# Performance work log

Measured on AMD Instinct MI355X. Metric: run time of the kernel, lower is better.

The kernel has to match this reference:

```python
import jax, jax.numpy as jnp
import numpy as np

B, L, C = 128, 512, 321
PRED = 336
S = 4
K = 25  # moving_avg kernel
EPS = 1e-5
N = L // S          # 128
H = 2048 // S       # 512


def setup_inputs() -> dict:
    key = jax.random.key(0)
    ks = jax.random.split(key, 16)
    def w(k, shape, fan_in):
        return jax.random.uniform(k, shape, jnp.float32, -1.0, 1.0) / np.sqrt(fan_in)
    return {
        "x": jax.random.normal(ks[0], (B, L, C), jnp.float32),
        "revin_w": jnp.ones((C,), jnp.float32),
        "revin_b": jnp.zeros((C,), jnp.float32),
        "W11": w(ks[1], (N, H), N), "b11": w(ks[2], (H,), N),
        "W12": w(ks[3], (H, N), H), "b12": w(ks[4], (N,), H),
        "W21": w(ks[5], (N, H), N), "b21": w(ks[6], (H,), N),
        "W22": w(ks[7], (H, N), H), "b22": w(ks[8], (N,), H),
        "W_tr": w(ks[9], (L, PRED), L), "b_tr": w(ks[10], (PRED,), L),
        "W_se": w(ks[11], (L, PRED), L), "b_se": w(ks[12], (PRED,), L),
    }


def reference(x, revin_w, revin_b, W11, b11, W12, b12, W21, b21, W22, b22,
              W_tr, b_tr, W_se, b_se):
    # RevIN norm (statistics are detached in the original)
    mean = jax.lax.stop_gradient(jnp.mean(x, axis=1, keepdims=True))
    std = jax.lax.stop_gradient(
        jnp.sqrt(jnp.var(x, axis=1, keepdims=True) + EPS))
    xn = (x - mean) / std * revin_w + revin_b  # [B, L, C]

    # Decomp: replicate-pad along time then moving average of width K
    front = jnp.repeat(xn[:, 0:1, :], K - 1 - (K - 1) // 2, axis=1)
    end = jnp.repeat(xn[:, -1:, :], (K - 1) // 2, axis=1)
    padded = jnp.concatenate([front, xn, end], axis=1)  # [B, L+K-1, C]
    cs = jnp.concatenate(
        [jnp.zeros((B, 1, C), padded.dtype), jnp.cumsum(padded, axis=1)], axis=1)
    trend = (cs[:, K:, :] - cs[:, :-K, :]) / K  # [B, L, C]
    seasonal = xn - trend

    trend_p = jnp.transpose(trend, (0, 2, 1))      # [B, C, L]
    seasonal_p = jnp.transpose(seasonal, (0, 2, 1))  # [B, C, L]

    # Trend head: Linear L -> PRED
    trend_out = jnp.einsum('bcl,lp->bcp', trend_p, W_tr) + b_tr

    # Seasonal head: Splitting (strided interleave) = reshape + transpose
    xs = seasonal_p.reshape(B, C, N, S).transpose(0, 1, 3, 2)  # [B, C, S, N]
    h = jnp.matmul(jax.nn.gelu(jnp.matmul(xs, W11) + b11, approximate=False), W12) + b12
    h = jnp.matmul(jax.nn.gelu(jnp.matmul(h, W21) + b21, approximate=False), W22) + b22
    # Catting is the exact inverse interleave
    sea = h.transpose(0, 1, 3, 2).reshape(B, C, L)  # [B, C, L]
    sea_out = jnp.einsum('bcl,lp->bcp', sea, W_se) + b_se

    out = jnp.transpose(trend_out + sea_out, (0, 2, 1))  # [B, PRED, C]

    # RevIN denorm
    out = (out - revin_b) / (revin_w + EPS * EPS)
    out = out * std + mean
    return out
```

## Files before the change

kernel.cpp:

```cpp
#include <hip/hip_runtime.h>
#include <math.h>

#define BB   128
#define LL   512
#define CC   321
#define PREDD 336

using bf16x8  = __attribute__((ext_vector_type(8))) __bf16;
using floatx4 = __attribute__((ext_vector_type(4))) float;
using uintx4  = __attribute__((ext_vector_type(4))) unsigned int;
typedef unsigned short u16;

__device__ __forceinline__ u16 f2bf(float f){
    union { float f; unsigned u; } v; v.f = f;
    unsigned r = v.u + 0x7FFFu + ((v.u >> 16) & 1u);
    return (u16)(r >> 16);
}

__device__ __forceinline__ float fgelu(float x){
    float u = x*(0.7978845608f + 0.035677408f*x*x);
    float a = fminf(u*2.8853900818f, 80.f);
    float t = __builtin_amdgcn_exp2f(a);
    return x*t*__builtin_amdgcn_rcpf(1.f + t);
}

__global__ void prep_k(const float* __restrict__ W11, const float* __restrict__ W12,
                       const float* __restrict__ W21, const float* __restrict__ W22,
                       const float* __restrict__ Wtr, const float* __restrict__ Wse,
                       u16* __restrict__ BT1, u16* __restrict__ BT2,
                       u16* __restrict__ BT3, u16* __restrict__ BT4,
                       u16* __restrict__ BT5)
{
    int idx = blockIdx.x * 256 + threadIdx.x;
    if (idx < 65536){
        int h = idx >> 7, k = idx & 127;
        BT1[idx] = f2bf(W11[k*512 + h]);
        BT3[idx] = f2bf(W21[k*512 + h]);
        int n = idx >> 9, k2 = idx & 511;
        BT2[idx] = f2bf(W12[k2*128 + n]);
        BT4[idx] = f2bf(W22[k2*128 + n]);
    }
    if (idx < 393216){
        int p = idx >> 10, k = idx & 1023;
        float v = 0.f;
        if (p < PREDD){
            if (k < 512) v = Wtr[k*PREDD + p];
            else { int kk = k - 512; int s = kk >> 7; int n = kk & 127; v = Wse[(4*n + s)*PREDD + p]; }
        }
        BT5[idx] = f2bf(v);
    }
}

#define XT(t,c) xt[((t)<<4) + (((t)>>5)<<1) + (c)]
__global__ __launch_bounds__(256) void decomp_k(
    const float* __restrict__ x, const float* __restrict__ rw, const float* __restrict__ rb,
    u16* __restrict__ Afin, u16* __restrict__ xs, float2* __restrict__ stats)
{
    __shared__ float xt[8240];
    __shared__ float red[2][16][16];
    __shared__ float sh_m[16], sh_istd[16];
    int b = blockIdx.x / 21, ct = blockIdx.x % 21;
    int tid = threadIdx.x;

    int cl = tid & 15, lp = tid >> 4;
    int c = ct*16 + cl;
    bool valid = c < CC;
    const float* xb = x + (size_t)b*LL*CC;
    float s = 0.f, q = 0.f;
    for (int i = 0; i < 32; ++i){
        int t = lp + 16*i;
        float v = valid ? xb[(size_t)t*CC + c] : 0.f;
        XT(t, cl) = v;
        s += v; q += v*v;
    }
    red[0][lp][cl] = s; red[1][lp][cl] = q;
    __syncthreads();
    if (tid < 16){
        float ss = 0.f, qq = 0.f;
        for (int j = 0; j < 16; ++j){ ss += red[0][j][tid]; qq += red[1][j][tid]; }
        float m  = ss * (1.f/512.f);
        float var = qq * (1.f/512.f) - m*m;
        float sd = sqrtf(var + 1e-5f);
        sh_m[tid] = m; sh_istd[tid] = 1.f/sd;
        int cc = ct*16 + tid;
        if (cc < CC) stats[(size_t)b*CC + cc] = make_float2(m, sd);
    }
    __syncthreads();

    int ch = tid >> 4, tp = tid & 15;
    int c2 = ct*16 + ch;
    if (c2 >= CC) return;
    float m = sh_m[ch], istd = sh_istd[ch];
    float w = rw[c2] * istd, bbv = rb[c2];
    size_t bc = (size_t)b*CC + c2;
    u16* tr  = Afin + bc*1024;
    u16* xsr = xs   + bc*512;
    int t0 = tp*32;

    float win = 0.f;
#pragma unroll
    for (int d = -12; d <= 12; ++d){
        int u = t0 + d; u = u < 0 ? 0 : (u > 511 ? 511 : u);
        win += XT(u, ch);
    }
    u16 trbuf[8];
    u16 xsbuf[4][8];
#pragma unroll
    for (int i = 0; i < 32; ++i){
        int t = t0 + i;
        float Ax = win * (1.f/25.f);
        float xv = XT(t, ch);
        trbuf[i & 7] = f2bf((Ax - m)*w + bbv);
        xsbuf[i & 3][i >> 2] = f2bf((xv - Ax)*w);
        if ((i & 7) == 7)
            *(uintx4*)(tr + t0 + (i & ~7)) = *(const uintx4*)trbuf;
        int uo = t - 12; uo = uo < 0 ? 0 : uo;
        int un = t + 13; un = un > 511 ? 511 : un;
        win += XT(un, ch) - XT(uo, ch);
    }
#pragma unroll
    for (int s4 = 0; s4 < 4; ++s4)
        *(uintx4*)(xsr + s4*128 + tp*8) = *(const uintx4*)xsbuf[s4];
}

#define SA 136
#define SB 72
#define HB0 8704
#define W2B0 17920
__global__ __launch_bounds__(256, 2) void mlp_fused_k(
    const u16* __restrict__ xs,
    const u16* __restrict__ BT1, const float* __restrict__ b11,
    const u16* __restrict__ BT2, const float* __restrict__ b12,
    const u16* __restrict__ BT3, const float* __restrict__ b21,
    const u16* __restrict__ BT4, const float* __restrict__ b22,
    u16* __restrict__ Afin)
{
    __shared__ u16 lds[27136];
    const int tid = threadIdx.x;
    const int row0 = blockIdx.x * 128;
    const int lane = tid & 63;
    const int wv = tid >> 6;
    const int wm = wv & 1, wn = wv >> 1;
    const int quad = lane >> 4, cl = lane & 15;

    {
        int r = tid >> 4, c8 = (tid & 15) * 8;
        const u16* src = xs + (size_t)(row0 + r)*128 + c8;
        u16* dst = lds + r*SA + c8;
#pragma unroll
        for (int p = 0; p < 8; ++p)
            *(uintx4*)(dst + p*16*SA) = *(const uintx4*)(src + (size_t)p*16*128);
    }
    __syncthreads();

    for (int mlp = 0; mlp < 2; ++mlp){
        const u16*  BTa = mlp ? BT3 : BT1;
        const float* ba = mlp ? b21 : b11;
        const u16*  BTb = mlp ? BT4 : BT2;
        const float* bb = mlp ? b22 : b12;

        bf16x8 afrag[4][4];
#pragma unroll
        for (int mt = 0; mt < 4; ++mt)
#pragma unroll
            for (int ks = 0; ks < 4; ++ks)
                afrag[mt][ks] = *(const bf16x8*)(lds + (wm*64 + mt*16 + cl)*SA + ks*32 + quad*8);
        __syncthreads();

        floatx4 Yacc[16];
#pragma unroll
        for (int i = 0; i < 16; ++i) Yacc[i] = (floatx4){0.f,0.f,0.f,0.f};

        for (int hc = 0; hc < 8; ++hc){
            {
                int r = tid >> 4, c8 = (tid & 15) * 8;
                const u16* src = BTa + (size_t)(hc*64 + r)*128 + c8;
                u16* dst = lds + r*SA + c8;
#pragma unroll
                for (int p = 0; p < 4; ++p)
                    *(uintx4*)(dst + p*16*SA) = *(const uintx4*)(src + (size_t)p*16*128);
            }
            __syncthreads();

            floatx4 hacc[8];
#pragma unroll
            for (int i = 0; i < 8; ++i) hacc[i] = (floatx4){0.f,0.f,0.f,0.f};
#pragma unroll
            for (int ks = 0; ks < 4; ++ks){
                bf16x8 bfr0 = *(const bf16x8*)(lds + (wn*32 +  0 + cl)*SA + ks*32 + quad*8);
                bf16x8 bfr1 = *(const bf16x8*)(lds + (wn*32 + 16 + cl)*SA + ks*32 + quad*8);
#pragma unroll
                for (int mt = 0; mt < 4; ++mt){
                    hacc[mt*2+0] = __builtin_amdgcn_mfma_f32_16x16x32_bf16(afrag[mt][ks], bfr0, hacc[mt*2+0], 0, 0, 0);
                    hacc[mt*2+1] = __builtin_amdgcn_mfma_f32_16x16x32_bf16(afrag[mt][ks], bfr1, hacc[mt*2+1], 0, 0, 0);
                }
            }
            {
                int hl0 = wn*32 + cl;
                float bav0 = ba[hc*64 + hl0];
                float bav1 = ba[hc*64 + hl0 + 16];
#pragma unroll
                for (int mt = 0; mt < 4; ++mt){
                    floatx4 v0 = hacc[mt*2+0], v1 = hacc[mt*2+1];
#pragma unroll
                    for (int i = 0; i < 4; ++i){
                        int r = wm*64 + mt*16 + quad*4 + i;
                        lds[HB0 + r*SB + hl0]      = f2bf(fgelu(v0[i] + bav0));
                        lds[HB0 + r*SB + hl0 + 16] = f2bf(fgelu(v1[i] + bav1));
                    }
                }
            }
            {
                int r = tid >> 3, c8 = (tid & 7) * 8;
                const u16* src = BTb + (size_t)r*512 + hc*64 + c8;
                u16* dst = lds + W2B0 + r*SB + c8;
#pragma unroll
                for (int p = 0; p < 4; ++p)
                    *(uintx4*)(dst + p*32*SB) = *(const uintx4*)(src + (size_t)p*32*512);
            }
            __syncthreads();

#pragma unroll
            for (int ks = 0; ks < 2; ++ks){
                bf16x8 a2[4], b2[4];
#pragma unroll
                for (int mt = 0; mt < 4; ++mt) a2[mt] = *(const bf16x8*)(lds + HB0  + (wm*64 + mt*16 + cl)*SB + ks*32 + quad*8);
#pragma unroll
                for (int nt = 0; nt < 4; ++nt) b2[nt] = *(const bf16x8*)(lds + W2B0 + (wn*64 + nt*16 + cl)*SB + ks*32 + quad*8);
#pragma unroll
                for (int mt = 0; mt < 4; ++mt)
#pragma unroll
                    for (int nt = 0; nt < 4; ++nt)
                        Yacc[mt*4+nt] = __builtin_amdgcn_mfma_f32_16x16x32_bf16(a2[mt], b2[nt], Yacc[mt*4+nt], 0, 0, 0);
            }
        }
        __syncthreads();

        if (mlp == 0){
#pragma unroll
            for (int mt = 0; mt < 4; ++mt)
#pragma unroll
                for (int nt = 0; nt < 4; ++nt){
                    int c = wn*64 + nt*16 + cl;
                    float bv = bb[c];
                    floatx4 v = Yacc[mt*4+nt];
#pragma unroll
                    for (int i = 0; i < 4; ++i){
                        int r = wm*64 + mt*16 + quad*4 + i;
                        lds[r*SA + c] = f2bf(v[i] + bv);
                    }
                }
            __syncthreads();
        } else {
#pragma unroll
            for (int mt = 0; mt < 4; ++mt)
#pragma unroll
                for (int nt = 0; nt < 4; ++nt){
                    int c = wn*64 + nt*16 + cl;
                    float bv = bb[c];
                    floatx4 v = Yacc[mt*4+nt];
#pragma unroll
                    for (int i = 0; i < 4; ++i){
                        int gr = row0 + wm*64 + mt*16 + quad*4 + i;
                        Afin[(size_t)(gr>>2)*1024 + 512 + (size_t)(gr&3)*128 + c] = f2bf(v[i] + bv);
                    }
                }
        }
    }
}

__global__ __launch_bounds__(256, 2) void head_gemm_k(
    const u16* __restrict__ A, const u16* __restrict__ BT,
    float* __restrict__ Cf,
    const float* __restrict__ bias, const float* __restrict__ bias2,
    const float* __restrict__ rw, const float* __restrict__ rb,
    const float2* __restrict__ stats)
{
    __shared__ u16 lA[128*72];
    __shared__ u16 lB[128*72];
    const int tid = threadIdx.x;
    const int row0 = blockIdx.y * 128;
    const int col0 = blockIdx.x * 128;
    const int lane = tid & 63;
    const int wv = tid >> 6;
    const int wm = wv & 1, wn = wv >> 1;
    const int quad = lane >> 4, cl = lane & 15;

    floatx4 acc[16];
#pragma unroll
    for (int i = 0; i < 16; ++i) acc[i] = (floatx4){0.f,0.f,0.f,0.f};

    const int srow = tid >> 3, sseg = tid & 7;
    const u16* Ag = A  + (size_t)(row0 + srow)*1024 + sseg*8;
    const u16* Bg = BT + (size_t)(col0 + srow)*1024 + sseg*8;

    for (int k0 = 0; k0 < 1024; k0 += 64){
#pragma unroll
        for (int p = 0; p < 4; ++p){
            uintx4 av = *(const uintx4*)(Ag + (size_t)p*32*1024 + k0);
            uintx4 bv = *(const uintx4*)(Bg + (size_t)p*32*1024 + k0);
            int r = p*32 + srow;
            *(uintx4*)(lA + r*72 + sseg*8) = av;
            *(uintx4*)(lB + r*72 + sseg*8) = bv;
        }
        __syncthreads();
#pragma unroll
        for (int kk = 0; kk < 2; ++kk){
            const int lk = kk*32 + quad*8;
            bf16x8 af[4], bfr[4];
#pragma unroll
            for (int mt = 0; mt < 4; ++mt) af[mt]  = *(const bf16x8*)(lA + (wm*64 + mt*16 + cl)*72 + lk);
#pragma unroll
            for (int nt = 0; nt < 4; ++nt) bfr[nt] = *(const bf16x8*)(lB + (wn*64 + nt*16 + cl)*72 + lk);
#pragma unroll
            for (int mt = 0; mt < 4; ++mt)
#pragma unroll
                for (int nt = 0; nt < 4; ++nt)
                    acc[mt*4+nt] = __builtin_amdgcn_mfma_f32_16x16x32_bf16(af[mt], bfr[nt], acc[mt*4+nt], 0, 0, 0);
        }
        __syncthreads();
    }

#pragma unroll
    for (int mt = 0; mt < 4; ++mt)
#pragma unroll
        for (int nt = 0; nt < 4; ++nt){
            floatx4 v = acc[mt*4+nt];
            int gc = col0 + wn*64 + nt*16 + cl;
            if (gc >= PREDD) continue;
            float bsum = bias[gc] + bias2[gc];
#pragma unroll
            for (int i = 0; i < 4; ++i){
                int gr = row0 + wm*64 + mt*16 + quad*4 + i;
                float val = v[i] + bsum;
                int bv2 = gr / CC;
                int c  = gr - bv2*CC;
                val = (val - rb[c]) / (rw[c] + 1e-10f);
                float2 st = stats[gr];
                val = val*st.y + st.x;
                Cf[(size_t)bv2*(PREDD*CC) + (size_t)gc*CC + c] = val;
            }
        }
}

extern "C" void kernel_launch(void* const* d_in, const int* in_sizes, int n_in,
                              void* d_out, int out_size, void* d_ws, size_t ws_size,
                              hipStream_t stream)
{
    const float* x   = (const float*)d_in[0];
    const float* rvw = (const float*)d_in[1];
    const float* rvb = (const float*)d_in[2];
    const float* W11 = (const float*)d_in[3];
    const float* b11 = (const float*)d_in[4];
    const float* W12 = (const float*)d_in[5];
    const float* b12 = (const float*)d_in[6];
    const float* W21 = (const float*)d_in[7];
    const float* b21 = (const float*)d_in[8];
    const float* W22 = (const float*)d_in[9];
    const float* b22 = (const float*)d_in[10];
    const float* Wtr = (const float*)d_in[11];
    const float* btr = (const float*)d_in[12];
    const float* Wse = (const float*)d_in[13];
    const float* bse = (const float*)d_in[14];
    float* out = (float*)d_out;

    char* ws = (char*)d_ws;
    u16* BT1 = (u16*)(ws + 0);
    u16* BT2 = (u16*)(ws + 131072);
    u16* BT3 = (u16*)(ws + 262144);
    u16* BT4 = (u16*)(ws + 393216);
    u16* BT5 = (u16*)(ws + 524288);
    float2* stats = (float2*)(ws + 1310720);
    u16* Afin = (u16*)(ws + 1639424);
    u16* xs   = (u16*)(ws + 85787648);

    hipLaunchKernelGGL(prep_k, dim3(1536), dim3(256), 0, stream,
                       W11, W12, W21, W22, Wtr, Wse, BT1, BT2, BT3, BT4, BT5);
    hipLaunchKernelGGL(decomp_k, dim3(128*21), dim3(256), 0, stream,
                       x, rvw, rvb, Afin, xs, stats);
    hipLaunchKernelGGL(mlp_fused_k, dim3(1284), dim3(256), 0, stream,
                       xs, BT1, b11, BT2, b12, BT3, b21, BT4, b22, Afin);
    hipLaunchKernelGGL(head_gemm_k, dim3(3, 321), dim3(256), 0, stream,
                       Afin, BT5, out, btr, bse, rvw, rvb, stats);
}
```

Measured before the change: 523.1 us.

## Software-pipeline weight loads and swizzle LDS in MLP and head GEMM kernels

The fused MLP kernel now prefetches the next hidden chunk's W1/W2 tiles into registers while computing. It double-buffers the GELU output and W2 tiles so the second GEMM of one chunk overlaps the first GEMM of the next. Padded LDS strides are replaced with XOR-swizzled layouts to avoid bank conflicts without padding. The head GEMM gets the same register prefetch and swizzle, with launch bounds raised to 3 blocks per CU, which adds register pressure and larger LDS use in the MLP kernel.

```diff
diff --git a/kernel.cpp b/kernel.cpp
--- a/kernel.cpp
+++ b/kernel.cpp
@@ -10,6 +10,8 @@
 using floatx4 = __attribute__((ext_vector_type(4))) float;
 using uintx4  = __attribute__((ext_vector_type(4))) unsigned int;
 typedef unsigned short u16;
+
+#define MFMA16(a,b,c) __builtin_amdgcn_mfma_f32_16x16x32_bf16(a,b,c,0,0,0)
 
 __device__ __forceinline__ u16 f2bf(float f){
     union { float f; unsigned u; } v; v.f = f;
@@ -23,6 +25,9 @@
     float t = __builtin_amdgcn_exp2f(a);
     return x*t*__builtin_amdgcn_rcpf(1.f + t);
 }
+
+__device__ __forceinline__ int swz128(int r, int s){ return r*128 + (((s & 8) | ((s ^ r) & 7)) << 3); }
+__device__ __forceinline__ int swz64 (int r, int s){ return r*64  + (((s ^ r) & 7) << 3); }
 
 __global__ void prep_k(const float* __restrict__ W11, const float* __restrict__ W12,
                        const float* __restrict__ W21, const float* __restrict__ W22,
@@ -123,10 +128,8 @@
         *(uintx4*)(xsr + s4*128 + tp*8) = *(const uintx4*)xsbuf[s4];
 }
 
-#define SA 136
-#define SB 72
-#define HB0 8704
-#define W2B0 17920
+#define W1B 16384
+#define W2B 24576
 __global__ __launch_bounds__(256, 2) void mlp_fused_k(
     const u16* __restrict__ xs,
     const u16* __restrict__ BT1, const float* __restrict__ b11,
@@ -135,7 +138,7 @@
     const u16* __restrict__ BT4, const float* __restrict__ b22,
     u16* __restrict__ Afin)
 {
-    __shared__ u16 lds[27136];
+    __shared__ u16 lds[40960];
     const int tid = threadIdx.x;
     const int row0 = blockIdx.x * 128;
     const int lane = tid & 63;
@@ -143,20 +146,26 @@
     const int wm = wv & 1, wn = wv >> 1;
     const int quad = lane >> 4, cl = lane & 15;
 
+    const int r1 = tid >> 2, s1 = tid & 3;
+    const int r2 = tid >> 1, s2 = (tid & 1)*4;
+
+    uintx4 w1r[4], w2r[4];
+#pragma unroll
+    for (int p = 0; p < 4; ++p){
+        w1r[p] = *(const uintx4*)(BT1 + (size_t)r1*128 + (s1 + 4*p)*8);
+        w2r[p] = *(const uintx4*)(BT2 + (size_t)r2*512 + (s2 + p)*8);
+    }
     {
-        int r = tid >> 4, c8 = (tid & 15) * 8;
-        const u16* src = xs + (size_t)(row0 + r)*128 + c8;
-        u16* dst = lds + r*SA + c8;
+        int rr = tid >> 4, seg = tid & 15;
+        const u16* src = xs + (size_t)(row0 + rr)*128 + seg*8;
 #pragma unroll
         for (int p = 0; p < 8; ++p)
-            *(uintx4*)(dst + p*16*SA) = *(const uintx4*)(src + (size_t)p*16*128);
+            *(uintx4*)(lds + swz128(rr + p*16, seg)) = *(const uintx4*)(src + (size_t)p*16*128);
     }
     __syncthreads();
 
     for (int mlp = 0; mlp < 2; ++mlp){
-        const u16*  BTa = mlp ? BT3 : BT1;
         const float* ba = mlp ? b21 : b11;
-        const u16*  BTb = mlp ? BT4 : BT2;
         const float* bb = mlp ? b22 : b12;
 
         bf16x8 afrag[4][4];
@@ -164,74 +173,105 @@
         for (int mt = 0; mt < 4; ++mt)
 #pragma unroll
             for (int ks = 0; ks < 4; ++ks)
-                afrag[mt][ks] = *(const bf16x8*)(lds + (wm*64 + mt*16 + cl)*SA + ks*32 + quad*8);
-        __syncthreads();
+                afrag[mt][ks] = *(const bf16x8*)(lds + swz128(wm*64 + mt*16 + cl, ks*4 + quad));
+
+        if (mlp == 0){
+#pragma unroll
+            for (int p = 0; p < 4; ++p){
+                *(uintx4*)(lds + W1B + swz128(r1, s1 + 4*p)) = w1r[p];
+                *(uintx4*)(lds + W2B + swz64(r2, s2 + p))    = w2r[p];
+            }
+        }
 
         floatx4 Yacc[16];
 #pragma unroll
         for (int i = 0; i < 16; ++i) Yacc[i] = (floatx4){0.f,0.f,0.f,0.f};
+        floatx4 hacc[8];
 
         for (int hc = 0; hc < 8; ++hc){
+            const int g = mlp*8 + hc;
+            __syncthreads();
+            if (g < 15){
+                const u16* w1s = ((g+1) & 8) ? BT3 : BT1;
+                const u16* w2s = ((g+1) & 8) ? BT4 : BT2;
+                const int hb = ((g+1) & 7) * 64;
+#pragma unroll
+                for (int p = 0; p < 4; ++p){
+                    w1r[p] = *(const uintx4*)(w1s + (size_t)(hb + r1)*128 + (s1 + 4*p)*8);
+                    w2r[p] = *(const uintx4*)(w2s + (size_t)r2*512 + hb + (s2 + p)*8);
+                }
+            }
+#pragma unroll
+            for (int i = 0; i < 8; ++i) hacc[i] = (floatx4){0.f,0.f,0.f,0.f};
+#pragma unroll
+            for (int ks = 0; ks < 4; ++ks){
+                bf16x8 b0 = *(const bf16x8*)(lds + W1B + swz128(wn*32 + cl,      ks*4 + quad));
+                bf16x8 b1 = *(const bf16x8*)(lds + W1B + swz128(wn*32 + 16 + cl, ks*4 + quad));
+#pragma unroll
+                for (int mt = 0; mt < 4; ++mt){
+                    hacc[mt*2+0] = MFMA16(afrag[mt][ks], b0, hacc[mt*2+0]);
+                    hacc[mt*2+1] = MFMA16(afrag[mt][ks], b1, hacc[mt*2+1]);
+                }
+            }
+            if (hc > 0){
+                const int HBp = ((hc-1) & 1) * 8192;
+                const int W2p = W2B + ((hc-1) & 1) * 8192;
+#pragma unroll
+                for (int ks = 0; ks < 2; ++ks){
+                    bf16x8 a2[4], b2[4];
+#pragma unroll
+                    for (int mt = 0; mt < 4; ++mt) a2[mt] = *(const bf16x8*)(lds + HBp + swz64(wm*64 + mt*16 + cl, ks*4 + quad));
+#pragma unroll
+                    for (int nt = 0; nt < 4; ++nt) b2[nt] = *(const bf16x8*)(lds + W2p + swz64(wn*64 + nt*16 + cl, ks*4 + quad));
+#pragma unroll
+                    for (int mt = 0; mt < 4; ++mt)
+#pragma unroll
+                        for (int nt = 0; nt < 4; ++nt)
+                            Yacc[mt*4+nt] = MFMA16(a2[mt], b2[nt], Yacc[mt*4+nt]);
+                }
+            }
             {
-                int r = tid >> 4, c8 = (tid & 15) * 8;
-                const u16* src = BTa + (size_t)(hc*64 + r)*128 + c8;
-                u16* dst = lds + r*SA + c8;
-#pragma unroll
-                for (int p = 0; p < 4; ++p)
-                    *(uintx4*)(dst + p*16*SA) = *(const uintx4*)(src + (size_t)p*16*128);
-            }
-            __syncthreads();
-
-            floatx4 hacc[8];
-#pragma unroll
-            for (int i = 0; i < 8; ++i) hacc[i] = (floatx4){0.f,0.f,0.f,0.f};
-#pragma unroll
-            for (int ks = 0; ks < 4; ++ks){
-                bf16x8 bfr0 = *(const bf16x8*)(lds + (wn*32 +  0 + cl)*SA + ks*32 + quad*8);
-                bf16x8 bfr1 = *(const bf16x8*)(lds + (wn*32 + 16 + cl)*SA + ks*32 + quad*8);
+                const int HB = (hc & 1) * 8192;
+                int h0 = wn*32 + cl;
+                int h1v = h0 + 16;
+                float bav0 = ba[hc*64 + h0];
+                float bav1 = ba[hc*64 + h1v];
 #pragma unroll
                 for (int mt = 0; mt < 4; ++mt){
-                    hacc[mt*2+0] = __builtin_amdgcn_mfma_f32_16x16x32_bf16(afrag[mt][ks], bfr0, hacc[mt*2+0], 0, 0, 0);
-                    hacc[mt*2+1] = __builtin_amdgcn_mfma_f32_16x16x32_bf16(afrag[mt][ks], bfr1, hacc[mt*2+1], 0, 0, 0);
-                }
-            }
-            {
-                int hl0 = wn*32 + cl;
-                float bav0 = ba[hc*64 + hl0];
-                float bav1 = ba[hc*64 + hl0 + 16];
-#pragma unroll
-                for (int mt = 0; mt < 4; ++mt){
-                    floatx4 v0 = hacc[mt*2+0], v1 = hacc[mt*2+1];
+                    floatx4 v0 = hacc[mt*2], v1 = hacc[mt*2+1];
 #pragma unroll
                     for (int i = 0; i < 4; ++i){
                         int r = wm*64 + mt*16 + quad*4 + i;
-                        lds[HB0 + r*SB + hl0]      = f2bf(fgelu(v0[i] + bav0));
-                        lds[HB0 + r*SB + hl0 + 16] = f2bf(fgelu(v1[i] + bav1));
+                        lds[HB + r*64 + (((h0 >> 3) ^ r) & 7)*8 + (h0 & 7)]  = f2bf(fgelu(v0[i] + bav0));
+                        lds[HB + r*64 + (((h1v >> 3) ^ r) & 7)*8 + (h1v & 7)] = f2bf(fgelu(v1[i] + bav1));
                     }
                 }
             }
-            {
-                int r = tid >> 3, c8 = (tid & 7) * 8;
-                const u16* src = BTb + (size_t)r*512 + hc*64 + c8;
-                u16* dst = lds + W2B0 + r*SB + c8;
-#pragma unroll
-                for (int p = 0; p < 4; ++p)
-                    *(uintx4*)(dst + p*32*SB) = *(const uintx4*)(src + (size_t)p*32*512);
-            }
             __syncthreads();
-
+            if (g < 15){
+#pragma unroll
+                for (int p = 0; p < 4; ++p){
+                    *(uintx4*)(lds + W1B + swz128(r1, s1 + 4*p))               = w1r[p];
+                    *(uintx4*)(lds + W2B + ((hc+1)&1)*8192 + swz64(r2, s2 + p)) = w2r[p];
+                }
+            }
+        }
+        __syncthreads();
+        {
+            const int HBp = 8192;
+            const int W2p = W2B + 8192;
 #pragma unroll
             for (int ks = 0; ks < 2; ++ks){
                 bf16x8 a2[4], b2[4];
 #pragma unroll
-                for (int mt = 0; mt < 4; ++mt) a2[mt] = *(const bf16x8*)(lds + HB0  + (wm*64 + mt*16 + cl)*SB + ks*32 + quad*8);
-#pragma unroll
-                for (int nt = 0; nt < 4; ++nt) b2[nt] = *(const bf16x8*)(lds + W2B0 + (wn*64 + nt*16 + cl)*SB + ks*32 + quad*8);
+                for (int mt = 0; mt < 4; ++mt) a2[mt] = *(const bf16x8*)(lds + HBp + swz64(wm*64 + mt*16 + cl, ks*4 + quad));
+#pragma unroll
+                for (int nt = 0; nt < 4; ++nt) b2[nt] = *(const bf16x8*)(lds + W2p + swz64(wn*64 + nt*16 + cl, ks*4 + quad));
 #pragma unroll
                 for (int mt = 0; mt < 4; ++mt)
 #pragma unroll
                     for (int nt = 0; nt < 4; ++nt)
-                        Yacc[mt*4+nt] = __builtin_amdgcn_mfma_f32_16x16x32_bf16(a2[mt], b2[nt], Yacc[mt*4+nt], 0, 0, 0);
+                        Yacc[mt*4+nt] = MFMA16(a2[mt], b2[nt], Yacc[mt*4+nt]);
             }
         }
         __syncthreads();
@@ -247,7 +287,7 @@
 #pragma unroll
                     for (int i = 0; i < 4; ++i){
                         int r = wm*64 + mt*16 + quad*4 + i;
-                        lds[r*SA + c] = f2bf(v[i] + bv);
+                        lds[r*128 + ((((c >> 3) & 8) | (((c >> 3) ^ r) & 7)) << 3) + (c & 7)] = f2bf(v[i] + bv);
                     }
                 }
             __syncthreads();
@@ -269,15 +309,15 @@
     }
 }
 
-__global__ __launch_bounds__(256, 2) void head_gemm_k(
+__global__ __launch_bounds__(256, 3) void head_gemm_k(
     const u16* __restrict__ A, const u16* __restrict__ BT,
     float* __restrict__ Cf,
     const float* __restrict__ bias, const float* __restrict__ bias2,
     const float* __restrict__ rw, const float* __restrict__ rb,
     const float2* __restrict__ stats)
 {
-    __shared__ u16 lA[128*72];
-    __shared__ u16 lB[128*72];
+    __shared__ u16 lA[8192];
+    __shared__ u16 lB[8192];
     const int tid = threadIdx.x;
     const int row0 = blockIdx.y * 128;
     const int col0 = blockIdx.x * 128;
@@ -290,33 +330,43 @@
 #pragma unroll
     for (int i = 0; i < 16; ++i) acc[i] = (floatx4){0.f,0.f,0.f,0.f};
 
-    const int srow = tid >> 3, sseg = tid & 7;
-    const u16* Ag = A  + (size_t)(row0 + srow)*1024 + sseg*8;
-    const u16* Bg = BT + (size_t)(col0 + srow)*1024 + sseg*8;
-
-    for (int k0 = 0; k0 < 1024; k0 += 64){
+    const int rs = tid >> 1, ss = (tid & 1)*4;
+    const u16* Ag = A  + (size_t)(row0 + rs)*1024 + ss*8;
+    const u16* Bg = BT + (size_t)(col0 + rs)*1024 + ss*8;
+
+    uintx4 arA[4], arB[4];
+#pragma unroll
+    for (int p = 0; p < 4; ++p){
+        arA[p] = *(const uintx4*)(Ag + p*8);
+        arB[p] = *(const uintx4*)(Bg + p*8);
+    }
+
+    for (int it = 0; it < 16; ++it){
 #pragma unroll
         for (int p = 0; p < 4; ++p){
-            uintx4 av = *(const uintx4*)(Ag + (size_t)p*32*1024 + k0);
-            uintx4 bv = *(const uintx4*)(Bg + (size_t)p*32*1024 + k0);
-            int r = p*32 + srow;
-            *(uintx4*)(lA + r*72 + sseg*8) = av;
-            *(uintx4*)(lB + r*72 + sseg*8) = bv;
+            *(uintx4*)(lA + swz64(rs, ss + p)) = arA[p];
+            *(uintx4*)(lB + swz64(rs, ss + p)) = arB[p];
         }
         __syncthreads();
+        if (it < 15){
+#pragma unroll
+            for (int p = 0; p < 4; ++p){
+                arA[p] = *(const uintx4*)(Ag + (it+1)*64 + p*8);
+                arB[p] = *(const uintx4*)(Bg + (it+1)*64 + p*8);
+            }
+        }
 #pragma unroll
         for (int kk = 0; kk < 2; ++kk){
-            const int lk = kk*32 + quad*8;
             bf16x8 af[4], bfr[4];
 #pragma unroll
-            for (int mt = 0; mt < 4; ++mt) af[mt]  = *(const bf16x8*)(lA + (wm*64 + mt*16 + cl)*72 + lk);
-#pragma unroll
-            for (int nt = 0; nt < 4; ++nt) bfr[nt] = *(const bf16x8*)(lB + (wn*64 + nt*16 + cl)*72 + lk);
+            for (int mt = 0; mt < 4; ++mt) af[mt]  = *(const bf16x8*)(lA + swz64(wm*64 + mt*16 + cl, kk*4 + quad));
+#pragma unroll
+            for (int nt = 0; nt < 4; ++nt) bfr[nt] = *(const bf16x8*)(lB + swz64(wn*64 + nt*16 + cl, kk*4 + quad));
 #pragma unroll
             for (int mt = 0; mt < 4; ++mt)
 #pragma unroll
                 for (int nt = 0; nt < 4; ++nt)
-                    acc[mt*4+nt] = __builtin_amdgcn_mfma_f32_16x16x32_bf16(af[mt], bfr[nt], acc[mt*4+nt], 0, 0, 0);
+                    acc[mt*4+nt] = MFMA16(af[mt], bfr[nt], acc[mt*4+nt]);
         }
         __syncthreads();
     }
```

Result: slower. 672.4 us (+28.5%).
